# Optimization experiments

Hardware: AMD Instinct MI355X
Metric: run time of the kernel (lower is better)

Reference implementation:

```python
import jax, jax.numpy as jnp
import numpy as np

B, L = 64, 512          # graphs, nodes per graph
N = B * L               # total nodes
INPUT_DIM, D, H, LAYERS, OUT = 128, 128, 8, 6, 10
DH = D // H
FF = 4 * D
E = 4 * N
SCALE = 0.02


def setup_inputs() -> dict:
    key = jax.random.key(0)
    ks = jax.random.split(key, 12)
    p = {}
    p['x'] = jax.random.normal(ks[0], (N, INPUT_DIM), jnp.float32)
    p['edge_index'] = jax.random.randint(ks[1], (2, E), 0, N, dtype=jnp.int64)
    p['batch'] = jnp.repeat(jnp.arange(B, dtype=jnp.int32), L)  # sorted graph ids
    p['max_nodes'] = L
    p['Wp'] = jax.random.normal(ks[2], (INPUT_DIM, D), jnp.float32) * SCALE
    p['bp'] = jnp.zeros((D,), jnp.float32)
    p['qkv_w'] = jax.random.normal(ks[3], (LAYERS, 3 * D, D), jnp.float32) * SCALE
    p['qkv_b'] = jnp.zeros((LAYERS, 3 * D), jnp.float32)
    p['out_w'] = jax.random.normal(ks[4], (LAYERS, D, D), jnp.float32) * SCALE
    p['out_b'] = jnp.zeros((LAYERS, D), jnp.float32)
    p['ln1_g'] = jnp.ones((LAYERS, D), jnp.float32)
    p['ln1_b'] = jnp.zeros((LAYERS, D), jnp.float32)
    p['ffn_w1'] = jax.random.normal(ks[5], (LAYERS, D, FF), jnp.float32) * SCALE
    p['ffn_b1'] = jnp.zeros((LAYERS, FF), jnp.float32)
    p['ffn_w2'] = jax.random.normal(ks[6], (LAYERS, FF, D), jnp.float32) * SCALE
    p['ffn_b2'] = jnp.zeros((LAYERS, D), jnp.float32)
    p['ln2_g'] = jnp.ones((LAYERS, D), jnp.float32)
    p['ln2_b'] = jnp.zeros((LAYERS, D), jnp.float32)
    p['cls_w1'] = jax.random.normal(ks[7], (D, D // 2), jnp.float32) * SCALE
    p['cls_b1'] = jnp.zeros((D // 2,), jnp.float32)
    p['cls_w2'] = jax.random.normal(ks[8], (D // 2, OUT), jnp.float32) * SCALE
    p['cls_b2'] = jnp.zeros((OUT,), jnp.float32)
    return p


def _ln(x, g, b, eps=1e-5):
    m = x.mean(-1, keepdims=True)
    v = ((x - m) ** 2).mean(-1, keepdims=True)
    return (x - m) * jax.lax.rsqrt(v + eps) * g + b


def _forward(x, batch, max_nodes, Wp, bp, qkv_w, qkv_b, out_w, out_b,
             ln1_g, ln1_b, ffn_w1, ffn_b1, ffn_w2, ffn_b2, ln2_g, ln2_b,
             cls_w1, cls_b1, cls_w2, cls_b2):
    n = x.shape[0]
    # --- vectorized ragged-to-dense (replaces the per-graph python loop) ---
    ones = jnp.ones((n,), jnp.int32)
    counts = jax.ops.segment_sum(ones, batch, num_segments=B)          # [B]
    starts = jnp.concatenate([jnp.zeros((1,), jnp.int32), jnp.cumsum(counts)[:-1]])
    pos = jnp.arange(n, dtype=jnp.int32) - starts[batch]               # slot within graph
    h0 = x @ Wp + bp                                                   # [N, D]
    h = jnp.zeros((B, max_nodes, D), h0.dtype).at[batch, pos].set(h0)  # [B, L, D]
    mask = jnp.zeros((B, max_nodes), bool).at[batch, pos].set(True)    # [B, L]
    # additive key-padding bias (src_key_padding_mask=~mask)
    bias = jnp.where(mask, 0.0, -1e9)[:, None, None, :]                # [B,1,1,L]
    inv_sqrt = 1.0 / np.sqrt(DH)
    for i in range(LAYERS):
        # --- post-norm MHA block ---
        qkv = jnp.einsum('bld,ed->ble', h, qkv_w[i]) + qkv_b[i]        # [B,L,3D]
        q, k, v = jnp.split(qkv, 3, axis=-1)
        q = q.reshape(B, max_nodes, H, DH).transpose(0, 2, 1, 3)       # [B,H,L,dh]
        k = k.reshape(B, max_nodes, H, DH).transpose(0, 2, 1, 3)
        v = v.reshape(B, max_nodes, H, DH).transpose(0, 2, 1, 3)
        scores = jnp.einsum('bhqd,bhkd->bhqk', q, k) * inv_sqrt + bias
        attn = jax.nn.softmax(scores, axis=-1)
        o = jnp.einsum('bhqk,bhkd->bhqd', attn, v)                     # [B,H,L,dh]
        o = o.transpose(0, 2, 1, 3).reshape(B, max_nodes, D)
        o = jnp.einsum('bld,ed->ble', o, out_w[i]) + out_b[i]
        h = _ln(h + o, ln1_g[i], ln1_b[i])
        # --- FFN block ---
        ff = jax.nn.relu(h @ ffn_w1[i] + ffn_b1[i]) @ ffn_w2[i] + ffn_b2[i]
        h = _ln(h + ff, ln2_g[i], ln2_b[i])
    # --- masked mean pooling per graph ---
    denom = jnp.maximum(counts.astype(h.dtype), 1.0)[:, None]          # [B,1]
    pooled = (h * mask[..., None].astype(h.dtype)).sum(axis=1) / denom # [B,D]
    # --- classifier head ---
    hid = jax.nn.relu(pooled @ cls_w1 + cls_b1)
    return hid @ cls_w2 + cls_b2                                       # [B,OUT]


def reference(x, edge_index, batch, max_nodes, Wp, bp, qkv_w, qkv_b, out_w, out_b,
              ln1_g, ln1_b, ffn_w1, ffn_b1, ffn_w2, ffn_b2, ln2_g, ln2_b,
              cls_w1, cls_b1, cls_w2, cls_b2):
    # edge_index is accepted (as in the torch module) but never used.
    return _forward(x, batch, max_nodes, Wp, bp, qkv_w, qkv_b, out_w, out_b,
                    ln1_g, ln1_b, ffn_w1, ffn_b1, ffn_w2, ffn_b2, ln2_g, ln2_b,
                    cls_w1, cls_b1, cls_w2, cls_b2)
```

## Files before the change

### kernel.cpp

```cpp
#include <hip/hip_runtime.h>
#include <hip/hip_bf16.h>


#define NROWS (64 * 512)
#define NLAYER 6

typedef __bf16 bf16x8 __attribute__((ext_vector_type(8)));
typedef float  f32x4  __attribute__((ext_vector_type(4)));
typedef float  f32x16 __attribute__((ext_vector_type(16)));

#define QSCALE 0.36067376022224085f

#if defined(__has_builtin)
#  if __has_builtin(__builtin_amdgcn_exp2f)
#    define FAST_EXP2(x) __builtin_amdgcn_exp2f(x)
#  endif
#endif
#ifndef FAST_EXP2
#  define FAST_EXP2(x) __expf((x) * 0.6931471805599453f)
#endif

__device__ __forceinline__ __hip_bfloat16 f2bf(float x) { return __float2bfloat16(x); }

__device__ __forceinline__ __hip_bfloat16 bf_rta(float a) {
  union { float f; unsigned u; } c{a};
  return __builtin_bit_cast(__hip_bfloat16, (unsigned short)((c.u + 0x8000u) >> 16));
}
__device__ __forceinline__ unsigned pk_rta(float a, float b) {
  union { float f; unsigned u; } ca{a}, cb{b};
  return ((ca.u + 0x8000u) >> 16) | ((cb.u + 0x8000u) & 0xFFFF0000u);
}

#define PN_X   (NROWS * 128)
#define PN_WP  (128 * 128)
#define PN_QW  (6 * 384 * 128)
#define PN_QB  (6 * 384)
#define PN_OW  (6 * 128 * 128)
#define PN_W1  (6 * 128 * 512)
#define PN_W2  (6 * 512 * 128)
#define PB1 PN_X
#define PB2 (PB1 + PN_WP)
#define PB3 (PB2 + PN_QW)
#define PB4 (PB3 + PN_QB)
#define PB5 (PB4 + PN_OW)
#define PB6 (PB5 + PN_W1)
#define PB7 (PB6 + PN_W2)

__global__ __launch_bounds__(256) void prep_kernel(
    const float* __restrict__ x, __hip_bfloat16* __restrict__ xb,
    const float* __restrict__ Wp, __hip_bfloat16* __restrict__ wp_t,
    const float* __restrict__ qkv_w, __hip_bfloat16* __restrict__ qkvw,
    const float* __restrict__ qkv_b, float* __restrict__ qb_s,
    const float* __restrict__ out_w, __hip_bfloat16* __restrict__ outw,
    const float* __restrict__ ffn_w1, __hip_bfloat16* __restrict__ w1t,
    const float* __restrict__ ffn_w2, __hip_bfloat16* __restrict__ w2t)
{
  const int idx = blockIdx.x * 256 + threadIdx.x;
  if (idx < PB1) {
    xb[idx] = f2bf(x[idx]);
  } else if (idx < PB2) {
    const int i = idx - PB1;
    const int c = i >> 7, r = i & 127;
    wp_t[i] = f2bf(Wp[r * 128 + c]);
  } else if (idx < PB3) {
    const int i = idx - PB2;
    const int row = (i >> 7) % 384;
    qkvw[i] = f2bf(qkv_w[i] * ((row < 128) ? QSCALE : 1.f));
  } else if (idx < PB4) {
    const int i = idx - PB3;
    qb_s[i] = qkv_b[i] * (((i % 384) < 128) ? QSCALE : 1.f);
  } else if (idx < PB5) {
    const int i = idx - PB4;
    outw[i] = f2bf(out_w[i]);
  } else if (idx < PB6) {
    const int i = idx - PB5;
    const int l = i >> 16, j = i & 65535;
    const int c = j >> 7, r = j & 127;
    w1t[i] = f2bf(ffn_w1[l * 65536 + r * 512 + c]);
  } else if (idx < PB7) {
    const int i = idx - PB6;
    const int l = i >> 16, j = i & 65535;
    const int c = j >> 9, r = j & 511;
    w2t[i] = f2bf(ffn_w2[l * 65536 + r * 128 + c]);
  }
}

__global__ __launch_bounds__(256) void gemm_fk(
    const __hip_bfloat16* __restrict__ A, const __hip_bfloat16* __restrict__ B,
    const float* __restrict__ bias, __hip_bfloat16* __restrict__ outb,
    __hip_bfloat16* __restrict__ hb,
    const float* __restrict__ lng, const float* __restrict__ lnb,
    int M, int K, int flags)
{
  __shared__ __align__(16) __hip_bfloat16 As[64 * 136];
  __shared__ __align__(16) __hip_bfloat16 Bs[128 * 136];

  const int tid = threadIdx.x;
  const int m0 = blockIdx.x << 6;
  const int wave = tid >> 6;
  const int lane = tid & 63;
  const int quad = lane >> 4;
  const int l15 = lane & 15;
  const int wrow = wave * 16;

  f32x4 acc[8];
#pragma unroll
  for (int ni = 0; ni < 8; ++ni) acc[ni] = (f32x4){0.f, 0.f, 0.f, 0.f};

  for (int kc = 0; kc < K; kc += 128) {
#pragma unroll
    for (int p = 0; p < 4; ++p) {
      const int e = tid + (p << 8);
      const int row = e >> 4;
      const int c = e & 15;
      *(uint4*)&As[row * 136 + c * 8] =
          *(const uint4*)(A + (size_t)(m0 + row) * K + kc + c * 8);
    }
#pragma unroll
    for (int p = 0; p < 8; ++p) {
      const int e = tid + (p << 8);
      const int row = e >> 4;
      const int c = e & 15;
      *(uint4*)&Bs[row * 136 + c * 8] =
          *(const uint4*)(B + (size_t)row * K + kc + c * 8);
    }
    __syncthreads();

#pragma unroll
    for (int ks = 0; ks < 4; ++ks) {
      const bf16x8 af = *(const bf16x8*)&As[(wrow + l15) * 136 + ks * 32 + quad * 8];
#pragma unroll
      for (int ni = 0; ni < 8; ++ni) {
        const bf16x8 bfr =
            *(const bf16x8*)&Bs[(ni * 16 + l15) * 136 + ks * 32 + quad * 8];
        acc[ni] = __builtin_amdgcn_mfma_f32_16x16x32_bf16(af, bfr, acc[ni], 0, 0, 0);
      }
    }
    if (kc + 128 < K) __syncthreads();
  }

  if (flags & 2) {
#pragma unroll
    for (int r = 0; r < 4; ++r) {
      const size_t row = (size_t)(m0 + wrow + quad * 4 + r);
      float s = 0.f, sq = 0.f;
#pragma unroll
      for (int ni = 0; ni < 8; ++ni) {
        const int cl = ni * 16 + l15;
        const float v = acc[ni][r] + bias[cl] +
                        __bfloat162float(hb[row * 128 + cl]);
        acc[ni][r] = v;
        s += v;
        sq += v * v;
      }
#pragma unroll
      for (int off = 1; off <= 8; off <<= 1) {
        s += __shfl_xor(s, off, 64);
        sq += __shfl_xor(sq, off, 64);
      }
      const float mean = s * (1.f / 128.f);
      const float var = sq * (1.f / 128.f) - mean * mean;
      const float rs = rsqrtf(var + 1e-5f);
#pragma unroll
      for (int ni = 0; ni < 8; ++ni) {
        const int cl = ni * 16 + l15;
        const float o = (acc[ni][r] - mean) * rs * lng[cl] + lnb[cl];
        hb[row * 128 + cl] = bf_rta(o);
      }
    }
  } else {
#pragma unroll
    for (int ni = 0; ni < 8; ++ni) {
      const int cl = ni * 16 + l15;
      const float bv = bias[cl];
#pragma unroll
      for (int r = 0; r < 4; ++r) {
        float v = acc[ni][r] + bv;
        if (flags & 1) v = fmaxf(v, 0.f);
        outb[(size_t)(m0 + wrow + quad * 4 + r) * 128 + cl] = bf_rta(v);
      }
    }
  }
}

__global__ __launch_bounds__(256) void ffn_fused(
    __hip_bfloat16* __restrict__ hb,
    const __hip_bfloat16* __restrict__ w1,
    const __hip_bfloat16* __restrict__ w2,
    const float* __restrict__ b1, const float* __restrict__ b2,
    const float* __restrict__ lng, const float* __restrict__ lnb)
{
  __shared__ __align__(16) __hip_bfloat16 AF[64 * 136];
  __shared__ __align__(16) __hip_bfloat16 Bs[128 * 136];

  const int tid = threadIdx.x;
  const int m0 = blockIdx.x << 6;
  const int wave = tid >> 6;
  const int lane = tid & 63;
  const int quad = lane >> 4;
  const int l15 = lane & 15;
  const int wrow = wave * 16;

#pragma unroll
  for (int p = 0; p < 4; ++p) {
    const int e = tid + (p << 8);
    const int row = e >> 4, c = e & 15;
    *(uint4*)&AF[row * 136 + c * 8] =
        *(const uint4*)(hb + (size_t)(m0 + row) * 128 + c * 8);
  }
#pragma unroll
  for (int p = 0; p < 8; ++p) {
    const int e = tid + (p << 8);
    const int row = e >> 4, c = e & 15;
    *(uint4*)&Bs[row * 136 + c * 8] =
        *(const uint4*)(w1 + (size_t)row * 128 + c * 8);
  }
  __syncthreads();

  bf16x8 af[4];
#pragma unroll
  for (int ks = 0; ks < 4; ++ks)
    af[ks] = *(const bf16x8*)&AF[(wrow + l15) * 136 + ks * 32 + quad * 8];

  f32x4 oacc[8];
#pragma unroll
  for (int ni = 0; ni < 8; ++ni) oacc[ni] = (f32x4){0.f, 0.f, 0.f, 0.f};

  for (int c = 0; c < 4; ++c) {
    if (c > 0) {
      __syncthreads();
#pragma unroll
      for (int p = 0; p < 8; ++p) {
        const int e = tid + (p << 8);
        const int row = e >> 4, cc = e & 15;
        *(uint4*)&Bs[row * 136 + cc * 8] =
            *(const uint4*)(w1 + (size_t)(c * 128 + row) * 128 + cc * 8);
      }
      __syncthreads();
    }

    f32x4 fc[8];
#pragma unroll
    for (int ni = 0; ni < 8; ++ni) fc[ni] = (f32x4){0.f, 0.f, 0.f, 0.f};
#pragma unroll
    for (int ks = 0; ks < 4; ++ks)
#pragma unroll
      for (int ni = 0; ni < 8; ++ni) {
        const bf16x8 wf =
            *(const bf16x8*)&Bs[(ni * 16 + l15) * 136 + ks * 32 + quad * 8];
        fc[ni] = __builtin_amdgcn_mfma_f32_16x16x32_bf16(wf, af[ks], fc[ni], 0, 0, 0);
      }
#pragma unroll
    for (int ni = 0; ni < 8; ++ni) {
      const f32x4 bv = *(const f32x4*)(b1 + c * 128 + ni * 16 + quad * 4);
      const float v0 = fmaxf(fc[ni][0] + bv[0], 0.f);
      const float v1 = fmaxf(fc[ni][1] + bv[1], 0.f);
      const float v2 = fmaxf(fc[ni][2] + bv[2], 0.f);
      const float v3 = fmaxf(fc[ni][3] + bv[3], 0.f);
      *(uint2*)&AF[(wrow + l15) * 136 + ni * 16 + quad * 4] =
          make_uint2(pk_rta(v0, v1), pk_rta(v2, v3));
    }
    __syncthreads();

#pragma unroll
    for (int p = 0; p < 8; ++p) {
      const int e = tid + (p << 8);
      const int row = e >> 4, cc = e & 15;
      *(uint4*)&Bs[row * 136 + cc * 8] =
          *(const uint4*)(w2 + (size_t)row * 512 + c * 128 + cc * 8);
    }
    __syncthreads();

#pragma unroll
    for (int ks2 = 0; ks2 < 4; ++ks2) {
      const bf16x8 ff =
          *(const bf16x8*)&AF[(wrow + l15) * 136 + ks2 * 32 + quad * 8];
#pragma unroll
      for (int ni = 0; ni < 8; ++ni) {
        const bf16x8 wf =
            *(const bf16x8*)&Bs[(ni * 16 + l15) * 136 + ks2 * 32 + quad * 8];
        oacc[ni] = __builtin_amdgcn_mfma_f32_16x16x32_bf16(ff, wf, oacc[ni], 0, 0, 0);
      }
    }
  }

#pragma unroll
  for (int r = 0; r < 4; ++r) {
    const size_t row = (size_t)(m0 + wrow + quad * 4 + r);
    float s = 0.f, sq = 0.f;
#pragma unroll
    for (int ni = 0; ni < 8; ++ni) {
      const int cl = ni * 16 + l15;
      const float v = oacc[ni][r] + b2[cl] + __bfloat162float(hb[row * 128 + cl]);
      oacc[ni][r] = v;
      s += v;
      sq += v * v;
    }
#pragma unroll
    for (int off = 1; off <= 8; off <<= 1) {
      s += __shfl_xor(s, off, 64);
      sq += __shfl_xor(sq, off, 64);
    }
    const float mean = s * (1.f / 128.f);
    const float var = sq * (1.f / 128.f) - mean * mean;
    const float rs = rsqrtf(var + 1e-5f);
#pragma unroll
    for (int ni = 0; ni < 8; ++ni) {
      const int cl = ni * 16 + l15;
      const float o = (oacc[ni][r] - mean) * rs * lng[cl] + lnb[cl];
      hb[row * 128 + cl] = bf_rta(o);
    }
  }
}

__global__ __launch_bounds__(512) void attn_kernel(
    const __hip_bfloat16* __restrict__ hbf,
    const __hip_bfloat16* __restrict__ qkvw_l,
    const float* __restrict__ qb_l,
    __hip_bfloat16* __restrict__ o)
{
  __shared__ __align__(16) __hip_bfloat16 Ks[512 * 24];
  __shared__ __align__(16) __hip_bfloat16 Vt[16 * 520];
  __shared__ __align__(16) __hip_bfloat16 PQ[8][1536];

  const int tid = threadIdx.x;
  const int b = blockIdx.x & 63;
  const int hh = blockIdx.x >> 6;
  const __hip_bfloat16* hrow = hbf + (size_t)b * 512 * 128;

  const int wave = tid >> 6;
  const int lane = tid & 63;
  const int l31 = lane & 31;
  const int l5 = lane >> 5;
  const int l15 = lane & 15;
  const int quad = lane >> 4;
  const int q0 = wave * 64;

  {
    f32x4 qacc[4], kacc[4], vacc[4];
#pragma unroll
    for (int mt = 0; mt < 4; ++mt) {
      qacc[mt] = (f32x4){0.f, 0.f, 0.f, 0.f};
      kacc[mt] = (f32x4){0.f, 0.f, 0.f, 0.f};
      vacc[mt] = (f32x4){0.f, 0.f, 0.f, 0.f};
    }
#pragma unroll
    for (int ks = 0; ks < 4; ++ks) {
      const int kc = ks * 32 + quad * 8;
      const bf16x8 wq = *(const bf16x8*)(qkvw_l + (size_t)(hh * 16 + l15) * 128 + kc);
      const bf16x8 wk = *(const bf16x8*)(qkvw_l + (size_t)(128 + hh * 16 + l15) * 128 + kc);
      const bf16x8 wv = *(const bf16x8*)(qkvw_l + (size_t)(256 + hh * 16 + l15) * 128 + kc);
#pragma unroll
      for (int mt = 0; mt < 4; ++mt) {
        const bf16x8 hf =
            *(const bf16x8*)(hrow + (size_t)(q0 + mt * 16 + l15) * 128 + kc);
        qacc[mt] = __builtin_amdgcn_mfma_f32_16x16x32_bf16(wq, hf, qacc[mt], 0, 0, 0);
        kacc[mt] = __builtin_amdgcn_mfma_f32_16x16x32_bf16(wk, hf, kacc[mt], 0, 0, 0);
        vacc[mt] = __builtin_amdgcn_mfma_f32_16x16x32_bf16(hf, wv, vacc[mt], 0, 0, 0);
      }
    }
    const f32x4 qb4 = *(const f32x4*)(qb_l + hh * 16 + quad * 4);
    const f32x4 kb4 = *(const f32x4*)(qb_l + 128 + hh * 16 + quad * 4);
    const float vbs = qb_l[256 + hh * 16 + l15];
#pragma unroll
    for (int mt = 0; mt < 4; ++mt) {
      *(uint2*)&PQ[wave][(mt * 16 + l15) * 24 + quad * 4] =
          make_uint2(pk_rta(qacc[mt][0] + qb4[0], qacc[mt][1] + qb4[1]),
                     pk_rta(qacc[mt][2] + qb4[2], qacc[mt][3] + qb4[3]));
      *(uint2*)&Ks[(q0 + mt * 16 + l15) * 24 + quad * 4] =
          make_uint2(pk_rta(kacc[mt][0] + kb4[0], kacc[mt][1] + kb4[1]),
                     pk_rta(kacc[mt][2] + kb4[2], kacc[mt][3] + kb4[3]));
      *(uint2*)&Vt[l15 * 520 + q0 + mt * 16 + quad * 4] =
          make_uint2(pk_rta(vacc[mt][0] + vbs, vacc[mt][1] + vbs),
                     pk_rta(vacc[mt][2] + vbs, vacc[mt][3] + vbs));
    }
  }

  bf16x8 qf[2];
#pragma unroll
  for (int s = 0; s < 2; ++s)
    qf[s] = *(const bf16x8*)&PQ[wave][(s * 32 + l31) * 24 + l5 * 8];
  __syncthreads();

  __hip_bfloat16* Pw = &PQ[wave][0];
  const f32x16 z16 = {};
  f32x4 oacc[2][2];
#pragma unroll
  for (int s = 0; s < 2; ++s) { oacc[s][0] = (f32x4){0.f,0.f,0.f,0.f};
                                oacc[s][1] = (f32x4){0.f,0.f,0.f,0.f}; }
  float lacc[2] = {0.f, 0.f};

  for (int kt = 0; kt < 16; ++kt) {
    const bf16x8 kf = *(const bf16x8*)&Ks[(kt * 32 + l31) * 24 + l5 * 8];
    const bf16x8 vf = *(const bf16x8*)&Vt[l15 * 520 + kt * 32 + quad * 8];
#pragma unroll
    for (int s = 0; s < 2; ++s) {
      f32x16 st = __builtin_amdgcn_mfma_f32_32x32x16_bf16(kf, qf[s], z16, 0, 0, 0);
      float pr[16];
#pragma unroll
      for (int r = 0; r < 16; ++r) pr[r] = FAST_EXP2(st[r]);
      const float s0 = (pr[0] + pr[1]) + (pr[2] + pr[3]);
      const float s1 = (pr[4] + pr[5]) + (pr[6] + pr[7]);
      const float s2 = (pr[8] + pr[9]) + (pr[10] + pr[11]);
      const float s3 = (pr[12] + pr[13]) + (pr[14] + pr[15]);
      lacc[s] += (s0 + s1) + (s2 + s3);
#pragma unroll
      for (int g = 0; g < 4; ++g) {
        *(uint2*)&Pw[l31 * 40 + g * 8 + l5 * 4] =
            make_uint2(pk_rta(pr[g * 4 + 0], pr[g * 4 + 1]),
                       pk_rta(pr[g * 4 + 2], pr[g * 4 + 3]));
      }
#pragma unroll
      for (int g = 0; g < 2; ++g) {
        const bf16x8 pf = *(const bf16x8*)&Pw[(g * 16 + l15) * 40 + quad * 8];
        oacc[s][g] = __builtin_amdgcn_mfma_f32_16x16x32_bf16(vf, pf, oacc[s][g], 0, 0, 0);
      }
    }
  }

#pragma unroll
  for (int s = 0; s < 2; ++s) {
    const float lv = lacc[s] + __shfl_xor(lacc[s], 32, 64);
#pragma unroll
    for (int g = 0; g < 2; ++g) {
      const float lq = __shfl(lv, g * 16 + l15, 64);
      const float inv = 1.f / lq;
      const int qrow = q0 + s * 32 + g * 16 + l15;
      *(uint2*)(o + ((size_t)b * 512 + qrow) * 128 + hh * 16 + quad * 4) =
          make_uint2(pk_rta(oacc[s][g][0] * inv, oacc[s][g][1] * inv),
                     pk_rta(oacc[s][g][2] * inv, oacc[s][g][3] * inv));
    }
  }
}

__global__ __launch_bounds__(256) void head_kernel(
    const __hip_bfloat16* __restrict__ h,
    const float* __restrict__ w1, const float* __restrict__ b1,
    const float* __restrict__ w2, const float* __restrict__ b2,
    float* __restrict__ out)
{
  __shared__ float part[2][128];
  __shared__ float pooled[128];
  __shared__ float hid[64];

  const int b = blockIdx.x;
  const int tid = threadIdx.x;
  const int d = tid & 127;
  const int half = tid >> 7;

  const __hip_bfloat16* hp = h + ((size_t)b * 512 + (size_t)half * 256) * 128;
  float s = 0.f;
  for (int r = 0; r < 256; ++r) s += __bfloat162float(hp[(size_t)r * 128 + d]);
  part[half][d] = s;
  __syncthreads();

  if (tid < 128) pooled[tid] = (part[0][tid] + part[1][tid]) * (1.f / 512.f);
  __syncthreads();

  if (tid < 64) {
    float a = b1[tid];
    for (int dd = 0; dd < 128; ++dd) a = fmaf(pooled[dd], w1[dd * 64 + tid], a);
    hid[tid] = fmaxf(a, 0.f);
  }
  __syncthreads();

  if (tid < 10) {
    float a = b2[tid];
    for (int j = 0; j < 64; ++j) a = fmaf(hid[j], w2[j * 10 + tid], a);
    out[b * 10 + tid] = a;
  }
}

extern "C" void kernel_launch(void* const* d_in, const int* in_sizes, int n_in,
                              void* d_out, int out_size, void* d_ws, size_t ws_size,
                              hipStream_t stream)
{
  (void)in_sizes; (void)n_in; (void)out_size; (void)ws_size;

  const float* x      = (const float*)d_in[0];
  const float* Wp     = (const float*)d_in[4];
  const float* bp     = (const float*)d_in[5];
  const float* qkv_w  = (const float*)d_in[6];
  const float* qkv_b  = (const float*)d_in[7];
  const float* out_w  = (const float*)d_in[8];
  const float* out_b  = (const float*)d_in[9];
  const float* ln1_g  = (const float*)d_in[10];
  const float* ln1_b  = (const float*)d_in[11];
  const float* ffn_w1 = (const float*)d_in[12];
  const float* ffn_b1 = (const float*)d_in[13];
  const float* ffn_w2 = (const float*)d_in[14];
  const float* ffn_b2 = (const float*)d_in[15];
  const float* ln2_g  = (const float*)d_in[16];
  const float* ln2_b  = (const float*)d_in[17];
  const float* cw1    = (const float*)d_in[18];
  const float* cb1    = (const float*)d_in[19];
  const float* cw2    = (const float*)d_in[20];
  const float* cb2    = (const float*)d_in[21];

  const int N = NROWS;

  __hip_bfloat16* hbf   = (__hip_bfloat16*)d_ws;
  __hip_bfloat16* xb    = hbf + (size_t)N * 128;
  __hip_bfloat16* attnb = xb + (size_t)N * 128;
  __hip_bfloat16* wp_t  = attnb + (size_t)N * 128;
  __hip_bfloat16* qkvw  = wp_t + 128 * 128;
  __hip_bfloat16* outw  = qkvw + 6 * 384 * 128;
  __hip_bfloat16* w1t   = outw + 6 * 128 * 128;
  __hip_bfloat16* w2t   = w1t + 6 * 512 * 128;
  float* qb_s = (float*)(w2t + 6 * 128 * 512);

  const dim3 blk(256);
  __hip_bfloat16* const nob = (__hip_bfloat16*)nullptr;
  const float* const nof = (const float*)nullptr;

  prep_kernel<<<dim3((PB7 + 255) / 256), blk, 0, stream>>>(
      x, xb, Wp, wp_t, qkv_w, qkvw, qkv_b, qb_s, out_w, outw,
      ffn_w1, w1t, ffn_w2, w2t);

  gemm_fk<<<dim3(N / 64), blk, 0, stream>>>(
      xb, wp_t, bp, hbf, nob, nof, nof, N, 128, 0);

  for (int i = 0; i < NLAYER; ++i) {
    attn_kernel<<<dim3(64 * 8), dim3(512), 0, stream>>>(
        hbf, qkvw + (size_t)i * 384 * 128, qb_s + (size_t)i * 384, attnb);

    gemm_fk<<<dim3(N / 64), blk, 0, stream>>>(
        attnb, outw + (size_t)i * 128 * 128, out_b + (size_t)i * 128,
        nob, hbf, ln1_g + (size_t)i * 128, ln1_b + (size_t)i * 128,
        N, 128, 2);

    ffn_fused<<<dim3(N / 64), blk, 0, stream>>>(
        hbf, w1t + (size_t)i * 512 * 128, w2t + (size_t)i * 128 * 512,
        ffn_b1 + (size_t)i * 512, ffn_b2 + (size_t)i * 128,
        ln2_g + (size_t)i * 128, ln2_b + (size_t)i * 128);
  }

  head_kernel<<<dim3(64), blk, 0, stream>>>(hbf, cw1, cb1, cw2, cb2, (float*)d_out);
}
```

Measured before the change: 516.2 us.

## Prefetch FFN weight chunks into registers and preload residuals before MMA

The FFN kernel now holds the next w1 and w2 weight chunks in registers while the current chunk is computed, so global loads overlap with MFMA work instead of sitting between barriers. Both the projection GEMM and the FFN kernel load the residual rows early (before compute or during the last chunk), which hides the latency of the epilogue reads. The projection GEMM also fixes K at compile time, drops its loop, and removes the unused ReLU flag. The cost is extra register pressure (w1r, w2r and hres arrays), which may lower occupancy.

Result: slower. 695.0 us (+34.6%).

```diff
diff --git a/kernel.cpp b/kernel.cpp
--- a/kernel.cpp
+++ b/kernel.cpp
@@ -90,8 +90,9 @@
     const float* __restrict__ bias, __hip_bfloat16* __restrict__ outb,
     __hip_bfloat16* __restrict__ hb,
     const float* __restrict__ lng, const float* __restrict__ lnb,
-    int M, int K, int flags)
+    int M, int flags)
 {
+  constexpr int K = 128;
   __shared__ __align__(16) __hip_bfloat16 As[64 * 136];
   __shared__ __align__(16) __hip_bfloat16 Bs[128 * 136];
 
@@ -102,41 +103,46 @@
   const int quad = lane >> 4;
   const int l15 = lane & 15;
   const int wrow = wave * 16;
+  const int srow = tid >> 4;
+  const int scol = tid & 15;
+
+#pragma unroll
+  for (int p = 0; p < 4; ++p) {
+    const int row = srow + p * 16;
+    *(uint4*)&As[row * 136 + scol * 8] =
+        *(const uint4*)(A + (size_t)(m0 + row) * K + scol * 8);
+  }
+#pragma unroll
+  for (int p = 0; p < 8; ++p) {
+    const int row = srow + p * 16;
+    *(uint4*)&Bs[row * 136 + scol * 8] =
+        *(const uint4*)(B + (size_t)row * K + scol * 8);
+  }
+
+  float hres[8][4];
+  if (flags & 2) {
+#pragma unroll
+    for (int ni = 0; ni < 8; ++ni)
+#pragma unroll
+      for (int r = 0; r < 4; ++r)
+        hres[ni][r] = __bfloat162float(
+            hb[(size_t)(m0 + wrow + quad * 4 + r) * 128 + ni * 16 + l15]);
+  }
+  __syncthreads();
 
   f32x4 acc[8];
 #pragma unroll
   for (int ni = 0; ni < 8; ++ni) acc[ni] = (f32x4){0.f, 0.f, 0.f, 0.f};
 
-  for (int kc = 0; kc < K; kc += 128) {
-#pragma unroll
-    for (int p = 0; p < 4; ++p) {
-      const int e = tid + (p << 8);
-      const int row = e >> 4;
-      const int c = e & 15;
-      *(uint4*)&As[row * 136 + c * 8] =
-          *(const uint4*)(A + (size_t)(m0 + row) * K + kc + c * 8);
-    }
-#pragma unroll
-    for (int p = 0; p < 8; ++p) {
-      const int e = tid + (p << 8);
-      const int row = e >> 4;
-      const int c = e & 15;
-      *(uint4*)&Bs[row * 136 + c * 8] =
-          *(const uint4*)(B + (size_t)row * K + kc + c * 8);
-    }
-    __syncthreads();
-
-#pragma unroll
-    for (int ks = 0; ks < 4; ++ks) {
-      const bf16x8 af = *(const bf16x8*)&As[(wrow + l15) * 136 + ks * 32 + quad * 8];
-#pragma unroll
-      for (int ni = 0; ni < 8; ++ni) {
-        const bf16x8 bfr =
-            *(const bf16x8*)&Bs[(ni * 16 + l15) * 136 + ks * 32 + quad * 8];
-        acc[ni] = __builtin_amdgcn_mfma_f32_16x16x32_bf16(af, bfr, acc[ni], 0, 0, 0);
-      }
-    }
-    if (kc + 128 < K) __syncthreads();
+#pragma unroll
+  for (int ks = 0; ks < 4; ++ks) {
+    const bf16x8 af = *(const bf16x8*)&As[(wrow + l15) * 136 + ks * 32 + quad * 8];
+#pragma unroll
+    for (int ni = 0; ni < 8; ++ni) {
+      const bf16x8 bfr =
+          *(const bf16x8*)&Bs[(ni * 16 + l15) * 136 + ks * 32 + quad * 8];
+      acc[ni] = __builtin_amdgcn_mfma_f32_16x16x32_bf16(af, bfr, acc[ni], 0, 0, 0);
+    }
   }
 
   if (flags & 2) {
@@ -146,9 +152,7 @@
       float s = 0.f, sq = 0.f;
 #pragma unroll
       for (int ni = 0; ni < 8; ++ni) {
-        const int cl = ni * 16 + l15;
-        const float v = acc[ni][r] + bias[cl] +
-                        __bfloat162float(hb[row * 128 + cl]);
+        const float v = acc[ni][r] + bias[ni * 16 + l15] + hres[ni][r];
         acc[ni][r] = v;
         s += v;
         sq += v * v;
@@ -174,11 +178,8 @@
       const int cl = ni * 16 + l15;
       const float bv = bias[cl];
 #pragma unroll
-      for (int r = 0; r < 4; ++r) {
-        float v = acc[ni][r] + bv;
-        if (flags & 1) v = fmaxf(v, 0.f);
-        outb[(size_t)(m0 + wrow + quad * 4 + r) * 128 + cl] = bf_rta(v);
-      }
+      for (int r = 0; r < 4; ++r)
+        outb[(size_t)(m0 + wrow + quad * 4 + r) * 128 + cl] = bf_rta(acc[ni][r] + bv);
     }
   }
 }
@@ -200,20 +201,21 @@
   const int quad = lane >> 4;
   const int l15 = lane & 15;
   const int wrow = wave * 16;
-
+  const int srow = tid >> 4;
+  const int scol = tid & 15;
+
+  uint4 w1r[8], w2r[8];
+#pragma unroll
+  for (int p = 0; p < 8; ++p) {
+    const int row = srow + p * 16;
+    w1r[p] = *(const uint4*)(w1 + (size_t)row * 128 + scol * 8);
+    w2r[p] = *(const uint4*)(w2 + (size_t)row * 512 + scol * 8);
+  }
 #pragma unroll
   for (int p = 0; p < 4; ++p) {
-    const int e = tid + (p << 8);
-    const int row = e >> 4, c = e & 15;
-    *(uint4*)&AF[row * 136 + c * 8] =
-        *(const uint4*)(hb + (size_t)(m0 + row) * 128 + c * 8);
-  }
-#pragma unroll
-  for (int p = 0; p < 8; ++p) {
-    const int e = tid + (p << 8);
-    const int row = e >> 4, c = e & 15;
-    *(uint4*)&Bs[row * 136 + c * 8] =
-        *(const uint4*)(w1 + (size_t)row * 128 + c * 8);
+    const int row = srow + p * 16;
+    *(uint4*)&AF[row * 136 + scol * 8] =
+        *(const uint4*)(hb + (size_t)(m0 + row) * 128 + scol * 8);
   }
   __syncthreads();
 
@@ -225,18 +227,19 @@
   f32x4 oacc[8];
 #pragma unroll
   for (int ni = 0; ni < 8; ++ni) oacc[ni] = (f32x4){0.f, 0.f, 0.f, 0.f};
+  float hres[8][4];
 
   for (int c = 0; c < 4; ++c) {
-    if (c > 0) {
-      __syncthreads();
-#pragma unroll
-      for (int p = 0; p < 8; ++p) {
-        const int e = tid + (p << 8);
-        const int row = e >> 4, cc = e & 15;
-        *(uint4*)&Bs[row * 136 + cc * 8] =
-            *(const uint4*)(w1 + (size_t)(c * 128 + row) * 128 + cc * 8);
-      }
-      __syncthreads();
+    if (c > 0) __syncthreads();
+#pragma unroll
+    for (int p = 0; p < 8; ++p)
+      *(uint4*)&Bs[(srow + p * 16) * 136 + scol * 8] = w1r[p];
+    __syncthreads();
+    if (c < 3) {
+#pragma unroll
+      for (int p = 0; p < 8; ++p)
+        w1r[p] = *(const uint4*)(
+            w1 + (size_t)((c + 1) * 128 + srow + p * 16) * 128 + scol * 8);
     }
 
     f32x4 fc[8];
@@ -261,15 +264,23 @@
           make_uint2(pk_rta(v0, v1), pk_rta(v2, v3));
     }
     __syncthreads();
-
-#pragma unroll
-    for (int p = 0; p < 8; ++p) {
-      const int e = tid + (p << 8);
-      const int row = e >> 4, cc = e & 15;
-      *(uint4*)&Bs[row * 136 + cc * 8] =
-          *(const uint4*)(w2 + (size_t)row * 512 + c * 128 + cc * 8);
-    }
+#pragma unroll
+    for (int p = 0; p < 8; ++p)
+      *(uint4*)&Bs[(srow + p * 16) * 136 + scol * 8] = w2r[p];
     __syncthreads();
+    if (c < 3) {
+#pragma unroll
+      for (int p = 0; p < 8; ++p)
+        w2r[p] = *(const uint4*)(
+            w2 + (size_t)(srow + p * 16) * 512 + (c + 1) * 128 + scol * 8);
+    } else {
+#pragma unroll
+      for (int ni = 0; ni < 8; ++ni)
+#pragma unroll
+        for (int r = 0; r < 4; ++r)
+          hres[ni][r] = __bfloat162float(
+              hb[(size_t)(m0 + wrow + quad * 4 + r) * 128 + ni * 16 + l15]);
+    }
 
 #pragma unroll
     for (int ks2 = 0; ks2 < 4; ++ks2) {
@@ -290,8 +301,7 @@
     float s = 0.f, sq = 0.f;
 #pragma unroll
     for (int ni = 0; ni < 8; ++ni) {
-      const int cl = ni * 16 + l15;
-      const float v = oacc[ni][r] + b2[cl] + __bfloat162float(hb[row * 128 + cl]);
+      const float v = oacc[ni][r] + b2[ni * 16 + l15] + hres[ni][r];
       oacc[ni][r] = v;
       s += v;
       sq += v * v;
@@ -518,7 +528,7 @@
       ffn_w1, w1t, ffn_w2, w2t);
 
   gemm_fk<<<dim3(N / 64), blk, 0, stream>>>(
-      xb, wp_t, bp, hbf, nob, nof, nof, N, 128, 0);
+      xb, wp_t, bp, hbf, nob, nof, nof, N, 0);
 
   for (int i = 0; i < NLAYER; ++i) {
     attn_kernel<<<dim3(64 * 8), dim3(512), 0, stream>>>(
@@ -527,7 +537,7 @@
     gemm_fk<<<dim3(N / 64), blk, 0, stream>>>(
         attnb, outw + (size_t)i * 128 * 128, out_b + (size_t)i * 128,
         nob, hbf, ln1_g + (size_t)i * 128, ln1_b + (size_t)i * 128,
-        N, 128, 2);
+        N, 2);
 
     ffn_fused<<<dim3(N / 64), blk, 0, stream>>>(
         hbf, w1t + (size_t)i * 512 * 128, w2t + (size_t)i * 128 * 512,
```
